# Performance work log

Measured on AMD Instinct MI355X. Metric: run time of the kernel, lower is better.

The kernel has to match this reference:

```python
import jax, jax.numpy as jnp
import numpy as np

B, S, D, H = 2, 2048, 512, 8
HD = D // H  # head_size = 64
EPS = 1e-5


def _layer_norm(x, g, b):
    m = jnp.mean(x, axis=-1, keepdims=True)
    v = jnp.mean(jnp.square(x - m), axis=-1, keepdims=True)
    return (x - m) * jax.lax.rsqrt(v + EPS) * g + b


def setup_inputs() -> dict:
    key = jax.random.key(0)
    ks = jax.random.split(key, 16)
    s_in = 1.0 / np.sqrt(D)
    s_ff = 1.0 / np.sqrt(4 * D)
    return {
        "x": jax.random.normal(ks[0], (B, S, D), jnp.float32),
        # per-head q/k/v projections stacked over heads: [H, D, HD]
        "Wq": jax.random.normal(ks[1], (H, D, HD), jnp.float32) * s_in,
        "bq": jax.random.normal(ks[2], (H, HD), jnp.float32) * s_in,
        "Wk": jax.random.normal(ks[3], (H, D, HD), jnp.float32) * s_in,
        "bk": jax.random.normal(ks[4], (H, HD), jnp.float32) * s_in,
        "Wv": jax.random.normal(ks[5], (H, D, HD), jnp.float32) * s_in,
        "bv": jax.random.normal(ks[6], (H, HD), jnp.float32) * s_in,
        "Wp": jax.random.normal(ks[7], (D, D), jnp.float32) * s_in,
        "bp": jax.random.normal(ks[8], (D,), jnp.float32) * s_in,
        "W1": jax.random.normal(ks[9], (D, 4 * D), jnp.float32) * s_in,
        "b1": jax.random.normal(ks[10], (4 * D,), jnp.float32) * s_in,
        "W2": jax.random.normal(ks[11], (4 * D, D), jnp.float32) * s_ff,
        "b2": jax.random.normal(ks[12], (D,), jnp.float32) * s_ff,
        "g1": jnp.ones((D,), jnp.float32),
        "be1": jnp.zeros((D,), jnp.float32),
        "g2": jnp.ones((D,), jnp.float32),
        "be2": jnp.zeros((D,), jnp.float32),
    }


def reference(x, Wq, bq, Wk, bk, Wv, bv, Wp, bp, W1, b1, W2, b2, g1, be1, g2, be2):
    # --- attention sublayer (pre-norm) ---
    xn = _layer_norm(x, g1, be1)                               # [B,S,D]
    q = jnp.einsum('bsd,hde->bhse', xn, Wq) + bq[None, :, None, :]
    k = jnp.einsum('bsd,hde->bhse', xn, Wk) + bk[None, :, None, :]
    v = jnp.einsum('bsd,hde->bhse', xn, Wv) + bv[None, :, None, :]
    # NOTE: original has NO 1/sqrt(head_size) scaling and NO mask
    scores = jnp.einsum('bhse,bhte->bhst', q, k)               # [B,H,S,S]
    w = jax.nn.softmax(scores, axis=-1)
    o = jnp.einsum('bhst,bhte->bhse', w, v)                    # [B,H,S,HD]
    o = o.transpose(0, 2, 1, 3).reshape(x.shape[0], x.shape[1], D)  # concat heads
    attn_out = o @ Wp + bp
    x = x + attn_out
    # --- MLP sublayer (pre-norm) ---
    xn2 = _layer_norm(x, g2, be2)
    h = jax.nn.relu(xn2 @ W1 + b1)
    x = x + (h @ W2 + b2)
    return x
```

## Files before the change

### kernel.cpp

```cpp
#include <hip/hip_runtime.h>
#include <hip/hip_bf16.h>

typedef unsigned short u16;
typedef unsigned long long u64t;
typedef __attribute__((ext_vector_type(8))) short bhalf8;
typedef __attribute__((ext_vector_type(4))) short bhalf4;
typedef __attribute__((ext_vector_type(4))) float f32x4;

#define MFMA16(a, b, c) __builtin_amdgcn_mfma_f32_16x16x32_bf16((a), (b), (c), 0, 0, 0)

#if __has_builtin(__builtin_amdgcn_mfma_f32_16x16x16bf16_1k)
#define HAVE_K16 1
#define MFMAK16(a, b, c) __builtin_amdgcn_mfma_f32_16x16x16bf16_1k((a), (b), (c), 0, 0, 0)
#elif __has_builtin(__builtin_amdgcn_mfma_f32_16x16x16_bf16)
#define HAVE_K16 1
#define MFMAK16(a, b, c) __builtin_amdgcn_mfma_f32_16x16x16_bf16((a), (b), (c), 0, 0, 0)
#else
#define HAVE_K16 0
#endif

#define BB 2
#define SS 2048
#define DD 512
#define HH 8
#define HD 64
#define NT (BB * SS)
#define LOG2E 1.44269504f

#if __has_builtin(__builtin_amdgcn_exp2f)
#define EXP2(x) __builtin_amdgcn_exp2f(x)
#else
#define EXP2(x) exp2f(x)
#endif

__device__ __forceinline__ u16 f2b(float f) {
    unsigned u = __builtin_bit_cast(unsigned, f);
    unsigned r = (u + 0x7fffu + ((u >> 16) & 1u)) >> 16;
    return (u16)r;
}

__device__ __forceinline__ void gl2lds16(const u16* g, u16* l) {
    u16* gn = (u16*)g;
    __builtin_amdgcn_global_load_lds((__attribute__((address_space(1))) void*)gn,
                                     (__attribute__((address_space(3))) void*)l, 16, 0, 0);
}

__global__ __launch_bounds__(256) void k_prep(const float* __restrict__ Wq, const float* __restrict__ Wk,
                                              const float* __restrict__ Wv, const float* __restrict__ Wp,
                                              const float* __restrict__ W1, const float* __restrict__ W2,
                                              const float* __restrict__ bq, const float* __restrict__ bk,
                                              const float* __restrict__ bv,
                                              u16* __restrict__ WqkvT, u16* __restrict__ WpT,
                                              u16* __restrict__ W1T, u16* __restrict__ W2T,
                                              float* __restrict__ biasqkv) {
    int j = blockIdx.x;
    int tx = threadIdx.x, ty = threadIdx.y;
    if (j >= 3072) {
        int i = (j - 3072) * 256 + ty * 32 + tx;
        biasqkv[i] = (i < 512) ? bq[i] : (i < 1024) ? bk[i - 512] : bv[i - 1024];
        return;
    }
    __shared__ float tile[32][33];
    const float* src; u16* dst; int R, C, tr, tc;
    if (j < 768) {
        int m = j >> 8, rem = j & 255, h = rem >> 5, tl = rem & 31;
        tr = tl >> 1; tc = tl & 1;
        src = (m == 0 ? Wq : (m == 1 ? Wk : Wv)) + h * 32768;
        dst = WqkvT + m * 262144 + h * 32768;
        R = 512; C = 64;
    } else if (j < 1024) { int tl = j - 768;  tr = tl >> 4; tc = tl & 15; src = Wp; dst = WpT; R = 512;  C = 512;  }
    else if (j < 2048)   { int tl = j - 1024; tr = tl >> 6; tc = tl & 63; src = W1; dst = W1T; R = 512;  C = 2048; }
    else                 { int tl = j - 2048; tr = tl >> 4; tc = tl & 15; src = W2; dst = W2T; R = 2048; C = 512;  }
    int c = tc * 32 + tx;
#pragma unroll
    for (int i = 0; i < 4; i++)
        tile[ty + i * 8][tx] = src[(size_t)(tr * 32 + ty + i * 8) * C + c];
    __syncthreads();
    int r2 = tr * 32 + tx;
#pragma unroll
    for (int i = 0; i < 4; i++)
        dst[(size_t)(tc * 32 + ty + i * 8) * R + r2] = f2b(tile[tx][ty + i * 8]);
}

__global__ __launch_bounds__(256) void k_layernorm(const float* __restrict__ x,
                                                   const float* __restrict__ g,
                                                   const float* __restrict__ be,
                                                   u16* __restrict__ out) {
    int wave = threadIdx.x >> 6, lane = threadIdx.x & 63;
    int row = blockIdx.x * 4 + wave;
    const float* xr = x + (size_t)row * DD;
    int c = lane * 8;
    float4 v0 = *(const float4*)(xr + c);
    float4 v1 = *(const float4*)(xr + c + 4);
    float s  = v0.x + v0.y + v0.z + v0.w + v1.x + v1.y + v1.z + v1.w;
    float sq = v0.x*v0.x + v0.y*v0.y + v0.z*v0.z + v0.w*v0.w
             + v1.x*v1.x + v1.y*v1.y + v1.z*v1.z + v1.w*v1.w;
#pragma unroll
    for (int m = 1; m < 64; m <<= 1) {
        s  += __shfl_xor(s, m);
        sq += __shfl_xor(sq, m);
    }
    float mean = s * (1.0f / DD);
    float var  = sq * (1.0f / DD) - mean * mean;
    float rstd = rsqrtf(var + 1e-5f);
    float4 g0 = *(const float4*)(g + c);
    float4 g1 = *(const float4*)(g + c + 4);
    float4 b0 = *(const float4*)(be + c);
    float4 b1 = *(const float4*)(be + c + 4);
    float xv[8] = {v0.x, v0.y, v0.z, v0.w, v1.x, v1.y, v1.z, v1.w};
    float gv[8] = {g0.x, g0.y, g0.z, g0.w, g1.x, g1.y, g1.z, g1.w};
    float bv[8] = {b0.x, b0.y, b0.z, b0.w, b1.x, b1.y, b1.z, b1.w};
    union { bhalf8 v; u16 u[8]; } pk;
#pragma unroll
    for (int i = 0; i < 8; i++) pk.u[i] = f2b((xv[i] - mean) * rstd * gv[i] + bv[i]);
    *(bhalf8*)(out + (size_t)row * DD + c) = pk.v;
}

template<int BM, int BN, int MI, int NI, int MODE>
__global__ __launch_bounds__(256) void k_gemm(const u16* __restrict__ A, const u16* __restrict__ Bt,
                                              const float* __restrict__ bias,
                                              int lda, int ldb, int kLen, int N,
                                              const float* __restrict__ resid,
                                              float* __restrict__ outF, u16* __restrict__ outB,
                                              u16* __restrict__ qd, u16* __restrict__ kd,
                                              u16* __restrict__ vtd) {
    constexpr int WM = MI * 16;
    constexpr int WN = NI * 16;
    static_assert(2 * WM == BM && 2 * WN == BN, "cfg");
    constexpr int ACH = BM / 4;
    constexpr int BCH = BN / 4;
    __shared__ u16 As[BM * 128];
    __shared__ u16 Bs[BN * 128];
    int t = threadIdx.x;
    int wave = t >> 6, lane = t & 63, quad = lane >> 4, l16 = lane & 15;
    int wr = wave >> 1, wc = wave & 1;
    int m0 = blockIdx.y * BM, n0 = blockIdx.x * BN;

    f32x4 acc[MI][NI] = {};

    int srow = lane >> 4;
    int scol = (lane & 15) * 8;
    const u16* Ag = A  + (size_t)(m0 + srow) * lda + scol;
    const u16* Bg = Bt + (size_t)(n0 + srow) * ldb + scol;

    for (int k0 = 0; k0 < kLen; k0 += 128) {
        __syncthreads();
#pragma unroll
        for (int c = 0; c < ACH / 4; c++) {
            int ch = wave * (ACH / 4) + c;
            gl2lds16(Ag + (size_t)(ch * 4) * lda + k0, &As[ch * 512]);
        }
#pragma unroll
        for (int c = 0; c < BCH / 4; c++) {
            int ch = wave * (BCH / 4) + c;
            gl2lds16(Bg + (size_t)(ch * 4) * ldb + k0, &Bs[ch * 512]);
        }
        __syncthreads();
#pragma unroll
        for (int h = 0; h < 4; h++) {
            bhalf8 af[MI], bf[NI];
#pragma unroll
            for (int mi = 0; mi < MI; mi++)
                af[mi] = *(bhalf8*)&As[(wr * WM + mi * 16 + l16) * 128 + h * 32 + quad * 8];
#pragma unroll
            for (int ni = 0; ni < NI; ni++)
                bf[ni] = *(bhalf8*)&Bs[(wc * WN + ni * 16 + l16) * 128 + h * 32 + quad * 8];
#pragma unroll
            for (int mi = 0; mi < MI; mi++)
#pragma unroll
                for (int ni = 0; ni < NI; ni++)
                    acc[mi][ni] = MFMA16(af[mi], bf[ni], acc[mi][ni]);
        }
    }

#pragma unroll
    for (int mi = 0; mi < MI; mi++)
#pragma unroll
        for (int ni = 0; ni < NI; ni++) {
            f32x4 a = acc[mi][ni];
            int gc = n0 + wc * WN + ni * 16 + l16;
            int gr0 = m0 + wr * WM + mi * 16 + quad * 4;
            float bsv = bias[gc];
            if (MODE == 0) {
                int mm = gc >> 9, cc = gc & 511;
                int hh = cc >> 6, e = cc & 63;
                int b = gr0 >> 11, s0 = gr0 & 2047;
                if (mm == 2) {
                    u64t pk = 0;
#pragma unroll
                    for (int r = 0; r < 4; r++) pk |= (u64t)f2b(a[r] + bsv) << (16 * r);
                    *(u64t*)&vtd[((size_t)(b * HH + hh) * HD + e) * SS + s0] = pk;
                } else if (mm == 0) {
#pragma unroll
                    for (int r = 0; r < 4; r++)
                        qd[((size_t)(b * HH + hh) * SS + s0 + r) * HD + e] = f2b((a[r] + bsv) * LOG2E);
                } else {
#pragma unroll
                    for (int r = 0; r < 4; r++)
                        kd[((size_t)(b * HH + hh) * SS + s0 + r) * HD + e] = f2b(a[r] + bsv);
                }
            } else if (MODE == 1) {
#pragma unroll
                for (int r = 0; r < 4; r++) {
                    size_t idx = (size_t)(gr0 + r) * N + gc;
                    outF[idx] = a[r] + bsv + resid[idx];
                }
            } else {
#pragma unroll
                for (int r = 0; r < 4; r++)
                    outB[(size_t)(gr0 + r) * N + gc] = f2b(fmaxf(a[r] + bsv, 0.0f));
            }
        }
}

__global__ __launch_bounds__(256) void k_attention(const u16* __restrict__ q,
                                                   const u16* __restrict__ k,
                                                   const u16* __restrict__ vt,
                                                   float* __restrict__ Opart,
                                                   float* __restrict__ lsum) {
    __shared__ u16 Ks[128 * 72];
    __shared__ u16 Vs[64 * 136];
    int bh = blockIdx.x, qt = blockIdx.y, kspl = blockIdx.z;
    int t = threadIdx.x, wave = t >> 6, lane = t & 63, quad = lane >> 4, l16 = lane & 15;
    const u16* qb = q  + (size_t)bh * SS * HD;
    const u16* kb = k  + (size_t)bh * SS * HD;
    const u16* vb = vt + (size_t)bh * HD * SS;

    bhalf8 qfa0, qfa1, qfb0, qfb1;
    {
        int r0 = qt * 128 + wave * 32 + l16;
        qfa0 = *(const bhalf8*)(qb + (size_t)r0 * HD + quad * 8);
        qfa1 = *(const bhalf8*)(qb + (size_t)r0 * HD + 32 + quad * 8);
        qfb0 = *(const bhalf8*)(qb + (size_t)(r0 + 16) * HD + quad * 8);
        qfb1 = *(const bhalf8*)(qb + (size_t)(r0 + 16) * HD + 32 + quad * 8);
    }

    f32x4 oacc[2][4] = {};
    float rsa = 0.f, rsb = 0.f;

    int kr = t >> 1, kc = (t & 1) * 32;
    int vr = t >> 2, vc = (t & 3) * 32;
    const u16* kp = kb + ((size_t)kspl * 1024 + kr) * HD + kc;
    const u16* vp = vb + (size_t)vr * SS + kspl * 1024 + vc;
    u16* ksd = &Ks[kr * 72 + kc];
    u16* vsd = &Vs[vr * 136 + vc];

    bhalf8 kreg[4], vreg[4];
#pragma unroll
    for (int i = 0; i < 4; i++) {
        kreg[i] = *(const bhalf8*)(kp + i * 8);
        vreg[i] = *(const bhalf8*)(vp + i * 8);
    }

    for (int it = 0; it < 8; it++) {
        __syncthreads();
#pragma unroll
        for (int i = 0; i < 4; i++) {
            *(bhalf8*)(ksd + i * 8) = kreg[i];
            *(bhalf8*)(vsd + i * 8) = vreg[i];
        }
        __syncthreads();
        if (it < 7) {
            const u16* kn = kp + (size_t)(it + 1) * 128 * HD;
            const u16* vn = vp + (it + 1) * 128;
#pragma unroll
            for (int i = 0; i < 4; i++) {
                kreg[i] = *(const bhalf8*)(kn + i * 8);
                vreg[i] = *(const bhalf8*)(vn + i * 8);
            }
        }

#pragma unroll
        for (int nt = 0; nt < 8; nt++) {
            bhalf8 kf0 = *(bhalf8*)&Ks[(nt * 16 + l16) * 72 + quad * 8];
            bhalf8 kf1 = *(bhalf8*)&Ks[(nt * 16 + l16) * 72 + 32 + quad * 8];
            f32x4 sa = {}, sb = {};
            sa = MFMA16(kf0, qfa0, sa);
            sa = MFMA16(kf1, qfa1, sa);
            sb = MFMA16(kf0, qfb0, sb);
            sb = MFMA16(kf1, qfb1, sb);
#if HAVE_K16
            union { bhalf4 v; u16 u[4]; } pa, pb;
#pragma unroll
            for (int r = 0; r < 4; r++) {
                float p0 = EXP2(sa[r]);
                float p1 = EXP2(sb[r]);
                rsa += p0; rsb += p1;
                pa.u[r] = f2b(p0); pb.u[r] = f2b(p1);
            }
#pragma unroll
            for (int et = 0; et < 4; et++) {
                bhalf4 vf = *(bhalf4*)&Vs[(et * 16 + l16) * 136 + nt * 16 + quad * 4];
                oacc[0][et] = MFMAK16(pa.v, vf, oacc[0][et]);
                oacc[1][et] = MFMAK16(pb.v, vf, oacc[1][et]);
            }
#else
            union { bhalf8 v; u16 u[8]; } pa, pb;
#pragma unroll
            for (int r = 0; r < 4; r++) {
                float p0 = EXP2(sa[r]);
                float p1 = EXP2(sb[r]);
                rsa += p0; rsb += p1;
                pa.u[r] = f2b(p0); pb.u[r] = f2b(p1);
            }
#pragma unroll
            for (int r = 4; r < 8; r++) { pa.u[r] = 0; pb.u[r] = 0; }
#pragma unroll
            for (int et = 0; et < 4; et++) {
                union { bhalf8 v; bhalf4 h[2]; } vf;
                vf.h[0] = *(bhalf4*)&Vs[(et * 16 + l16) * 136 + nt * 16 + quad * 4];
                vf.h[1] = (bhalf4){0, 0, 0, 0};
                oacc[0][et] = MFMA16(pa.v, vf.v, oacc[0][et]);
                oacc[1][et] = MFMA16(pb.v, vf.v, oacc[1][et]);
            }
#endif
        }
    }

    rsa += __shfl_xor(rsa, 16); rsa += __shfl_xor(rsa, 32);
    rsb += __shfl_xor(rsb, 16); rsb += __shfl_xor(rsb, 32);

#pragma unroll
    for (int qc = 0; qc < 2; qc++) {
        int sbase = qt * 128 + wave * 32 + qc * 16;
        float* Ob = Opart + ((size_t)(kspl * 16 + bh) * SS + sbase) * HD;
#pragma unroll
        for (int et = 0; et < 4; et++)
#pragma unroll
            for (int r = 0; r < 4; r++)
                Ob[(quad * 4 + r) * HD + et * 16 + l16] = oacc[qc][et][r];
        if (quad == 0)
            lsum[(size_t)(kspl * 16 + bh) * SS + sbase + l16] = (qc == 0 ? rsa : rsb);
    }
}

__global__ __launch_bounds__(256) void k_combine(const float* __restrict__ Opart,
                                                 const float* __restrict__ lsum,
                                                 u16* __restrict__ oc) {
    int tid = blockIdx.x * 256 + threadIdx.x;
    int c4 = tid & 15, s = (tid >> 4) & 2047, bh = tid >> 15;
    size_t i0 = ((size_t)bh * SS + s) * HD + c4 * 4;
    float4 p0 = *(const float4*)(Opart + i0);
    float4 p1 = *(const float4*)(Opart + (size_t)16 * SS * HD + i0);
    float l = lsum[(size_t)bh * SS + s] + lsum[(size_t)16 * SS + (size_t)bh * SS + s];
    float inv = 1.0f / l;
    u64t pk = 0;
    pk |= (u64t)f2b((p0.x + p1.x) * inv);
    pk |= (u64t)f2b((p0.y + p1.y) * inv) << 16;
    pk |= (u64t)f2b((p0.z + p1.z) * inv) << 32;
    pk |= (u64t)f2b((p0.w + p1.w) * inv) << 48;
    int b = bh >> 3, h = bh & 7;
    *(u64t*)&oc[((size_t)b * SS + s) * DD + h * HD + c4 * 4] = pk;
}

extern "C" void kernel_launch(void* const* d_in, const int* in_sizes, int n_in,
                              void* d_out, int out_size, void* d_ws, size_t ws_size,
                              hipStream_t stream) {
    const float* x   = (const float*)d_in[0];
    const float* Wq  = (const float*)d_in[1];
    const float* bq  = (const float*)d_in[2];
    const float* Wk  = (const float*)d_in[3];
    const float* bk  = (const float*)d_in[4];
    const float* Wv  = (const float*)d_in[5];
    const float* bv  = (const float*)d_in[6];
    const float* Wp  = (const float*)d_in[7];
    const float* bp  = (const float*)d_in[8];
    const float* W1  = (const float*)d_in[9];
    const float* b1  = (const float*)d_in[10];
    const float* W2  = (const float*)d_in[11];
    const float* b2  = (const float*)d_in[12];
    const float* g1  = (const float*)d_in[13];
    const float* be1 = (const float*)d_in[14];
    const float* g2  = (const float*)d_in[15];
    const float* be2 = (const float*)d_in[16];

    char* ws = (char*)d_ws;
    u16*   WqkvT   = (u16*)(ws + 0);
    u16*   WpT     = (u16*)(ws + 1572864);
    u16*   W1T     = (u16*)(ws + 2097152);
    u16*   W2T     = (u16*)(ws + 4194304);
    float* biasqkv = (float*)(ws + 6291456);
    u16*   xn      = (u16*)(ws + 6297600);
    u16*   qB      = (u16*)(ws + 10491904);
    u16*   kB      = (u16*)(ws + 14686208);
    u16*   vTb     = (u16*)(ws + 18880512);
    u16*   oc      = (u16*)(ws + 23074816);
    float* x1      = (float*)(ws + 27269120);
    u16*   xn2     = (u16*)(ws + 35657728);
    u16*   hbuf    = (u16*)(ws + 39852032);
    float* Opart   = (float*)hbuf;
    float* lsum    = (float*)xn;

    k_prep<<<3078, dim3(32, 8), 0, stream>>>(Wq, Wk, Wv, Wp, W1, W2, bq, bk, bv,
                                             WqkvT, WpT, W1T, W2T, biasqkv);
    k_layernorm<<<NT / 4, 256, 0, stream>>>(x, g1, be1, xn);
    k_gemm<64, 128, 2, 4, 0><<<dim3(12, 64), 256, 0, stream>>>(
        xn, WqkvT, biasqkv, 512, 512, 512, 1536, nullptr, nullptr, nullptr, qB, kB, vTb);
    k_attention<<<dim3(16, 16, 2), 256, 0, stream>>>(qB, kB, vTb, Opart, lsum);
    k_combine<<<2048, 256, 0, stream>>>(Opart, lsum, oc);
    k_gemm<64, 64, 2, 2, 1><<<dim3(8, 64), 256, 0, stream>>>(
        oc, WpT, bp, 512, 512, 512, 512, x, x1, nullptr, nullptr, nullptr, nullptr);
    k_layernorm<<<NT / 4, 256, 0, stream>>>(x1, g2, be2, xn2);
    k_gemm<64, 128, 2, 4, 2><<<dim3(16, 64), 256, 0, stream>>>(
        xn2, W1T, b1, 512, 512, 512, 2048, nullptr, nullptr, hbuf, nullptr, nullptr, nullptr);
    k_gemm<64, 64, 2, 2, 1><<<dim3(8, 64), 256, 0, stream>>>(
        hbuf, W2T, b2, 2048, 2048, 2048, 512, x1, (float*)d_out, nullptr, nullptr, nullptr, nullptr);
}
```

Measured before the change: 233.4 us.

## Retile GEMMs with K=64 chunks and split attention KV tiles across two wave groups

The GEMM kernel now uses a configurable wave grid and a 64-wide K chunk, which halves shared memory per tile. The QKV and MLP-up GEMMs move to larger 128x128 tiles. Attention blocks grow to 512 threads, with two wave groups each handling half of every 128-key tile; their partial outputs and row sums are then reduced through shared memory. The aim is more parallelism per block and more data reuse, at the cost of extra syncs, an LDS reduction, and fewer GEMM blocks.

```diff
diff --git a/kernel.cpp b/kernel.cpp
--- a/kernel.cpp
+++ b/kernel.cpp
@@ -116,7 +116,7 @@
     *(bhalf8*)(out + (size_t)row * DD + c) = pk.v;
 }
 
-template<int BM, int BN, int MI, int NI, int MODE>
+template<int BM, int BN, int WR, int WC, int MI, int NI, int MODE>
 __global__ __launch_bounds__(256) void k_gemm(const u16* __restrict__ A, const u16* __restrict__ Bt,
                                               const float* __restrict__ bias,
                                               int lda, int ldb, int kLen, int N,
@@ -126,45 +126,48 @@
                                               u16* __restrict__ vtd) {
     constexpr int WM = MI * 16;
     constexpr int WN = NI * 16;
-    static_assert(2 * WM == BM && 2 * WN == BN, "cfg");
-    constexpr int ACH = BM / 4;
-    constexpr int BCH = BN / 4;
-    __shared__ u16 As[BM * 128];
-    __shared__ u16 Bs[BN * 128];
+    static_assert(WR * WM == BM && WC * WN == BN && WR * WC == 4, "cfg");
+    constexpr int ACH = BM / 32;
+    constexpr int BCH = BN / 32;
+    __shared__ u16 As[BM * 64];
+    __shared__ u16 Bs[BN * 64];
     int t = threadIdx.x;
     int wave = t >> 6, lane = t & 63, quad = lane >> 4, l16 = lane & 15;
-    int wr = wave >> 1, wc = wave & 1;
+    int wr, wc;
+    if (WC == 1)      { wr = wave; wc = 0; }
+    else if (WR == 1) { wr = 0;    wc = wave; }
+    else              { wr = wave >> 1; wc = wave & 1; }
     int m0 = blockIdx.y * BM, n0 = blockIdx.x * BN;
 
     f32x4 acc[MI][NI] = {};
 
-    int srow = lane >> 4;
-    int scol = (lane & 15) * 8;
+    int srow = lane >> 3;
+    int scol = (lane & 7) * 8;
     const u16* Ag = A  + (size_t)(m0 + srow) * lda + scol;
     const u16* Bg = Bt + (size_t)(n0 + srow) * ldb + scol;
 
-    for (int k0 = 0; k0 < kLen; k0 += 128) {
+    for (int k0 = 0; k0 < kLen; k0 += 64) {
         __syncthreads();
 #pragma unroll
-        for (int c = 0; c < ACH / 4; c++) {
-            int ch = wave * (ACH / 4) + c;
-            gl2lds16(Ag + (size_t)(ch * 4) * lda + k0, &As[ch * 512]);
-        }
-#pragma unroll
-        for (int c = 0; c < BCH / 4; c++) {
-            int ch = wave * (BCH / 4) + c;
-            gl2lds16(Bg + (size_t)(ch * 4) * ldb + k0, &Bs[ch * 512]);
+        for (int c = 0; c < ACH; c++) {
+            int ch = wave * ACH + c;
+            gl2lds16(Ag + (size_t)(ch * 8) * lda + k0, &As[ch * 512]);
+        }
+#pragma unroll
+        for (int c = 0; c < BCH; c++) {
+            int ch = wave * BCH + c;
+            gl2lds16(Bg + (size_t)(ch * 8) * ldb + k0, &Bs[ch * 512]);
         }
         __syncthreads();
 #pragma unroll
-        for (int h = 0; h < 4; h++) {
+        for (int h = 0; h < 2; h++) {
             bhalf8 af[MI], bf[NI];
 #pragma unroll
             for (int mi = 0; mi < MI; mi++)
-                af[mi] = *(bhalf8*)&As[(wr * WM + mi * 16 + l16) * 128 + h * 32 + quad * 8];
+                af[mi] = *(bhalf8*)&As[(wr * WM + mi * 16 + l16) * 64 + h * 32 + quad * 8];
 #pragma unroll
             for (int ni = 0; ni < NI; ni++)
-                bf[ni] = *(bhalf8*)&Bs[(wc * WN + ni * 16 + l16) * 128 + h * 32 + quad * 8];
+                bf[ni] = *(bhalf8*)&Bs[(wc * WN + ni * 16 + l16) * 64 + h * 32 + quad * 8];
 #pragma unroll
             for (int mi = 0; mi < MI; mi++)
 #pragma unroll
@@ -213,22 +216,27 @@
         }
 }
 
-__global__ __launch_bounds__(256) void k_attention(const u16* __restrict__ q,
+__global__ __launch_bounds__(512) void k_attention(const u16* __restrict__ q,
                                                    const u16* __restrict__ k,
                                                    const u16* __restrict__ vt,
                                                    float* __restrict__ Opart,
                                                    float* __restrict__ lsum) {
-    __shared__ u16 Ks[128 * 72];
-    __shared__ u16 Vs[64 * 136];
+    __shared__ u16 sm[17920];
+    u16* Ks = sm;
+    u16* Vs = sm + 9216;
+    float* Ored = (float*)sm;
+    float* Lred = (float*)sm + 8192;
+
     int bh = blockIdx.x, qt = blockIdx.y, kspl = blockIdx.z;
     int t = threadIdx.x, wave = t >> 6, lane = t & 63, quad = lane >> 4, l16 = lane & 15;
+    int g = wave >> 2, qw = wave & 3;
     const u16* qb = q  + (size_t)bh * SS * HD;
     const u16* kb = k  + (size_t)bh * SS * HD;
     const u16* vb = vt + (size_t)bh * HD * SS;
 
     bhalf8 qfa0, qfa1, qfb0, qfb1;
     {
-        int r0 = qt * 128 + wave * 32 + l16;
+        int r0 = qt * 128 + qw * 32 + l16;
         qfa0 = *(const bhalf8*)(qb + (size_t)r0 * HD + quad * 8);
         qfa1 = *(const bhalf8*)(qb + (size_t)r0 * HD + 32 + quad * 8);
         qfb0 = *(const bhalf8*)(qb + (size_t)(r0 + 16) * HD + quad * 8);
@@ -238,16 +246,16 @@
     f32x4 oacc[2][4] = {};
     float rsa = 0.f, rsb = 0.f;
 
-    int kr = t >> 1, kc = (t & 1) * 32;
-    int vr = t >> 2, vc = (t & 3) * 32;
+    int kr = t >> 2, kc = (t & 3) * 16;
+    int vr = t >> 3, vc = (t & 7) * 16;
     const u16* kp = kb + ((size_t)kspl * 1024 + kr) * HD + kc;
     const u16* vp = vb + (size_t)vr * SS + kspl * 1024 + vc;
     u16* ksd = &Ks[kr * 72 + kc];
     u16* vsd = &Vs[vr * 136 + vc];
 
-    bhalf8 kreg[4], vreg[4];
-#pragma unroll
-    for (int i = 0; i < 4; i++) {
+    bhalf8 kreg[2], vreg[2];
+#pragma unroll
+    for (int i = 0; i < 2; i++) {
         kreg[i] = *(const bhalf8*)(kp + i * 8);
         vreg[i] = *(const bhalf8*)(vp + i * 8);
     }
@@ -255,7 +263,7 @@
     for (int it = 0; it < 8; it++) {
         __syncthreads();
 #pragma unroll
-        for (int i = 0; i < 4; i++) {
+        for (int i = 0; i < 2; i++) {
             *(bhalf8*)(ksd + i * 8) = kreg[i];
             *(bhalf8*)(vsd + i * 8) = vreg[i];
         }
@@ -264,14 +272,15 @@
             const u16* kn = kp + (size_t)(it + 1) * 128 * HD;
             const u16* vn = vp + (it + 1) * 128;
 #pragma unroll
-            for (int i = 0; i < 4; i++) {
+            for (int i = 0; i < 2; i++) {
                 kreg[i] = *(const bhalf8*)(kn + i * 8);
                 vreg[i] = *(const bhalf8*)(vn + i * 8);
             }
         }
 
 #pragma unroll
-        for (int nt = 0; nt < 8; nt++) {
+        for (int nt2 = 0; nt2 < 4; nt2++) {
+            int nt = g * 4 + nt2;
             bhalf8 kf0 = *(bhalf8*)&Ks[(nt * 16 + l16) * 72 + quad * 8];
             bhalf8 kf1 = *(bhalf8*)&Ks[(nt * 16 + l16) * 72 + 32 + quad * 8];
             f32x4 sa = {}, sb = {};
@@ -320,17 +329,38 @@
     rsa += __shfl_xor(rsa, 16); rsa += __shfl_xor(rsa, 32);
     rsb += __shfl_xor(rsb, 16); rsb += __shfl_xor(rsb, 32);
 
-#pragma unroll
-    for (int qc = 0; qc < 2; qc++) {
-        int sbase = qt * 128 + wave * 32 + qc * 16;
-        float* Ob = Opart + ((size_t)(kspl * 16 + bh) * SS + sbase) * HD;
-#pragma unroll
-        for (int et = 0; et < 4; et++)
-#pragma unroll
-            for (int r = 0; r < 4; r++)
-                Ob[(quad * 4 + r) * HD + et * 16 + l16] = oacc[qc][et][r];
-        if (quad == 0)
-            lsum[(size_t)(kspl * 16 + bh) * SS + sbase + l16] = (qc == 0 ? rsa : rsb);
+    __syncthreads();
+    if (g == 1) {
+#pragma unroll
+        for (int qc = 0; qc < 2; qc++)
+#pragma unroll
+            for (int et = 0; et < 4; et++)
+#pragma unroll
+                for (int r = 0; r < 4; r++)
+                    Ored[(qw * 32 + qc * 16 + quad * 4 + r) * 64 + et * 16 + l16] = oacc[qc][et][r];
+        if (quad == 0) {
+            Lred[qw * 32 + l16]      = rsa;
+            Lred[qw * 32 + 16 + l16] = rsb;
+        }
+    }
+    __syncthreads();
+    if (g == 0) {
+#pragma unroll
+        for (int qc = 0; qc < 2; qc++) {
+            int sbase = qt * 128 + qw * 32 + qc * 16;
+            float* Ob = Opart + ((size_t)(kspl * 16 + bh) * SS + sbase) * HD;
+#pragma unroll
+            for (int et = 0; et < 4; et++)
+#pragma unroll
+                for (int r = 0; r < 4; r++) {
+                    float v = oacc[qc][et][r]
+                            + Ored[(qw * 32 + qc * 16 + quad * 4 + r) * 64 + et * 16 + l16];
+                    Ob[(quad * 4 + r) * HD + et * 16 + l16] = v;
+                }
+            if (quad == 0)
+                lsum[(size_t)(kspl * 16 + bh) * SS + sbase + l16] =
+                    (qc == 0 ? rsa : rsb) + Lred[qw * 32 + qc * 16 + l16];
+        }
     }
 }
 
@@ -394,15 +424,15 @@
     k_prep<<<3078, dim3(32, 8), 0, stream>>>(Wq, Wk, Wv, Wp, W1, W2, bq, bk, bv,
                                              WqkvT, WpT, W1T, W2T, biasqkv);
     k_layernorm<<<NT / 4, 256, 0, stream>>>(x, g1, be1, xn);
-    k_gemm<64, 128, 2, 4, 0><<<dim3(12, 64), 256, 0, stream>>>(
+    k_gemm<128, 128, 2, 2, 4, 4, 0><<<dim3(12, 32), 256, 0, stream>>>(
         xn, WqkvT, biasqkv, 512, 512, 512, 1536, nullptr, nullptr, nullptr, qB, kB, vTb);
-    k_attention<<<dim3(16, 16, 2), 256, 0, stream>>>(qB, kB, vTb, Opart, lsum);
+    k_attention<<<dim3(16, 16, 2), 512, 0, stream>>>(qB, kB, vTb, Opart, lsum);
     k_combine<<<2048, 256, 0, stream>>>(Opart, lsum, oc);
-    k_gemm<64, 64, 2, 2, 1><<<dim3(8, 64), 256, 0, stream>>>(
+    k_gemm<64, 64, 2, 2, 2, 2, 1><<<dim3(8, 64), 256, 0, stream>>>(
         oc, WpT, bp, 512, 512, 512, 512, x, x1, nullptr, nullptr, nullptr, nullptr);
     k_layernorm<<<NT / 4, 256, 0, stream>>>(x1, g2, be2, xn2);
-    k_gemm<64, 128, 2, 4, 2><<<dim3(16, 64), 256, 0, stream>>>(
+    k_gemm<128, 128, 2, 2, 4, 4, 2><<<dim3(16, 32), 256, 0, stream>>>(
         xn2, W1T, b1, 512, 512, 512, 2048, nullptr, nullptr, hbuf, nullptr, nullptr, nullptr);
-    k_gemm<64, 64, 2, 2, 1><<<dim3(8, 64), 256, 0, stream>>>(
+    k_gemm<64, 64, 2, 2, 2, 2, 1><<<dim3(8, 64), 256, 0, stream>>>(
         hbuf, W2T, b2, 2048, 2048, 2048, 512, x1, (float*)d_out, nullptr, nullptr, nullptr, nullptr);
 }
```

Measured after the change: 209.5 us. 10.3% less time.
